# Kernel tuning notes

Hardware: AMD Instinct MI355X
Metric: run time of the kernel (lower is better)

Reference implementation:

```python
import jax, jax.numpy as jnp
import numpy as np

B, S, H = 2, 2048, 1024
NUM_HEAD = 16
HEAD = H // NUM_HEAD
NEG = -10000000000.0


def setup_inputs() -> dict:
    key = jax.random.key(0)
    ks = jax.random.split(key, 10)
    scale = 1.0 / np.sqrt(H)
    return {
        "query": jax.random.normal(ks[0], (B, S, H), jnp.float32),
        "key": jax.random.normal(ks[1], (B, S, H), jnp.float32),
        "value": jax.random.normal(ks[2], (B, S, H), jnp.float32),
        "mask": jax.random.randint(ks[3], (B, S), 0, 2, jnp.int32),
        "Wq": jax.random.normal(ks[4], (H, H), jnp.float32) * scale,
        "bq": jnp.zeros((H,), jnp.float32),
        "Wk": jax.random.normal(ks[5], (H, H), jnp.float32) * scale,
        "bk": jnp.zeros((H,), jnp.float32),
        "Wv": jax.random.normal(ks[6], (H, H), jnp.float32) * scale,
        "bv": jnp.zeros((H,), jnp.float32),
    }


def reference(query, key, value, mask, Wq, bq, Wk, bk, Wv, bv):
    b, s, h = query.shape
    # Linear projections (torch Linear: x @ W.T + b), split into heads -> [b, nh, s, hd]
    def proj(x, W, bias):
        y = x @ W.T + bias
        return y.reshape(b, s, NUM_HEAD, HEAD).transpose(0, 2, 1, 3)

    q = proj(query, Wq, bq)
    k = proj(key, Wk, bk)
    v = proj(value, Wv, bv)

    # NOTE: original module has NO 1/sqrt(head_dim) scaling -- faithful.
    attn_score = jnp.einsum("bhqd,bhkd->bhqk", q, k)  # [b, nh, s, s]
    # key-padding mask bias: 0 where mask==1, -1e10 where mask==0, broadcast over query dim
    bias_add = jnp.where(mask[:, None, None, :] == 0, NEG, 0.0).astype(attn_score.dtype)
    attn_score = attn_score + bias_add
    attn_ratio = jax.nn.softmax(attn_score, axis=-1)
    out = jnp.einsum("bhqk,bhkd->bhqd", attn_ratio, v)  # [b, nh, s, hd]
    out = out.transpose(0, 2, 1, 3).reshape(b, s, h)
    # Dropout is identity in eval mode; output_linear is defined but never used in forward.
    return out
```

## Files before the change

kernel.cpp:

```cpp
#include <hip/hip_runtime.h>

#define BATCH 2
#define S_LEN 2048
#define HDIM  1024
#define NHEAD 16
#define HD    64
#define NEGBIAS -1e10f
#define LOG2E 1.44269504088896f

typedef __attribute__((ext_vector_type(8))) _Float16 half8;
typedef __attribute__((ext_vector_type(4))) _Float16 half4;
typedef __attribute__((ext_vector_type(4))) float   f32x4;
typedef __attribute__((ext_vector_type(2))) __fp16 fp16x2;
typedef __attribute__((ext_vector_type(4))) __fp16 fp16x4;
typedef __attribute__((ext_vector_type(8))) __fp16 fp16x8;

__device__ __forceinline__ float max3f(float a, float b, float c) {
    return fmaxf(fmaxf(a, b), c);
}

__global__ __launch_bounds__(256) void proj_gemm_f16(
    const float* __restrict__ Xq, const float* __restrict__ Wq, const float* __restrict__ bq,
    const float* __restrict__ Xk, const float* __restrict__ Wk, const float* __restrict__ bk,
    const float* __restrict__ Xv, const float* __restrict__ Wv, const float* __restrict__ bv,
    _Float16* __restrict__ Qb, _Float16* __restrict__ Kb, _Float16* __restrict__ Vtb)
{
    const int z = blockIdx.z;
    const float* X    = (z == 0) ? Xq : (z == 1) ? Xk : Xv;
    const float* W    = (z == 0) ? Wq : (z == 1) ? Wk : Wv;
    const float* bias = (z == 0) ? bq : (z == 1) ? bk : bv;
    _Float16* Y       = (z == 0) ? Qb : (z == 1) ? Kb : Vtb;

    const int n0 = blockIdx.x * 128;
    const int m0 = blockIdx.y * 128;

    __shared__ __align__(16) _Float16 As[128][40];
    __shared__ __align__(16) _Float16 Bs[128][40];

    const int t    = threadIdx.x;
    const int w    = t >> 6;
    const int lane = t & 63;
    const int quad = lane >> 4;
    const int lc   = lane & 15;
    const int wm   = (w >> 1) * 64;
    const int wn   = (w & 1) * 64;

    const f32x4 fzero = {0.f, 0.f, 0.f, 0.f};
    f32x4 acc[4][4];
#pragma unroll
    for (int i = 0; i < 4; i++)
#pragma unroll
        for (int j = 0; j < 4; j++) acc[i][j] = fzero;

    const int srow = t >> 2;
    const int sc   = t & 3;

    float4 xa[2][2], wa[2][2];
#define PROJ_ISSUE(K0)                                                        \
    {                                                                         \
        _Pragma("unroll")                                                     \
        for (int hf = 0; hf < 2; hf++) {                                      \
            const float* gx = X + (size_t)(m0 + srow + hf * 64) * HDIM + (K0) + sc * 8; \
            xa[hf][0] = *(const float4*)gx;                                   \
            xa[hf][1] = *(const float4*)(gx + 4);                             \
            const float* gw = W + (size_t)(n0 + srow + hf * 64) * HDIM + (K0) + sc * 8; \
            wa[hf][0] = *(const float4*)gw;                                   \
            wa[hf][1] = *(const float4*)(gw + 4);                             \
        }                                                                     \
    }

#define PK8(dst, f0, f1)                                                      \
    {                                                                         \
        fp16x2 p0 = __builtin_amdgcn_cvt_pkrtz((f0).x, (f0).y);               \
        fp16x2 p1 = __builtin_amdgcn_cvt_pkrtz((f0).z, (f0).w);               \
        fp16x2 p2 = __builtin_amdgcn_cvt_pkrtz((f1).x, (f1).y);               \
        fp16x2 p3 = __builtin_amdgcn_cvt_pkrtz((f1).z, (f1).w);               \
        fp16x4 lo = __builtin_shufflevector(p0, p1, 0, 1, 2, 3);              \
        fp16x4 hi = __builtin_shufflevector(p2, p3, 0, 1, 2, 3);              \
        fp16x8 v8 = __builtin_shufflevector(lo, hi, 0, 1, 2, 3, 4, 5, 6, 7);  \
        dst = __builtin_bit_cast(half8, v8);                                  \
    }

    PROJ_ISSUE(0)

    for (int k0 = 0; k0 < HDIM; k0 += 32) {
        if (k0) __syncthreads();
#pragma unroll
        for (int hf = 0; hf < 2; hf++) {
            int row = srow + hf * 64;
            half8 vx, vw;
            PK8(vx, xa[hf][0], xa[hf][1])
            PK8(vw, wa[hf][0], wa[hf][1])
            *(half8*)&As[row][sc * 8] = vx;
            *(half8*)&Bs[row][sc * 8] = vw;
        }
        __syncthreads();

        if (k0 + 32 < HDIM) PROJ_ISSUE(k0 + 32)

        half8 af[4], bf[4];
#pragma unroll
        for (int mt = 0; mt < 4; mt++)
            af[mt] = *(const half8*)&As[wm + mt * 16 + lc][quad * 8];
#pragma unroll
        for (int nt = 0; nt < 4; nt++)
            bf[nt] = *(const half8*)&Bs[wn + nt * 16 + lc][quad * 8];
#pragma unroll
        for (int mt = 0; mt < 4; mt++)
#pragma unroll
            for (int nt = 0; nt < 4; nt++)
                acc[mt][nt] = __builtin_amdgcn_mfma_f32_16x16x32_f16(
                    af[mt], bf[nt], acc[mt][nt], 0, 0, 0);
    }

#pragma unroll
    for (int nt = 0; nt < 4; nt++) {
        const int n = n0 + wn + nt * 16 + lc;
        const float bv_ = bias[n];
        const int h = n >> 6, d = n & 63;
#pragma unroll
        for (int mt = 0; mt < 4; mt++) {
#pragma unroll
            for (int r = 0; r < 4; r++) {
                const int m = m0 + wm + mt * 16 + quad * 4 + r;
                const int b = m >> 11, s = m & (S_LEN - 1);
                const int bh = b * NHEAD + h;
                float y = acc[mt][nt][r] + bv_;
                if (z == 0) y *= LOG2E;
                _Float16 val = (_Float16)y;
                if (z == 2)
                    Y[((size_t)bh * HD + d) * S_LEN + s] = val;
                else
                    Y[((size_t)bh * S_LEN + s) * HD + d] = val;
            }
        }
    }
}

__global__ __launch_bounds__(256) void flash_attn_mfma(
    const _Float16* __restrict__ Qb, const _Float16* __restrict__ Kb,
    const _Float16* __restrict__ Vtb, const int* __restrict__ mask,
    float* __restrict__ out)
{
    const int bid = blockIdx.x;
    const int swz = (bid & 7) * 64 + (bid >> 3);
    const int qt = swz & 15;
    const int bh = swz >> 4;
    const int b  = bh >> 4;
    const int h  = bh & (NHEAD - 1);

    __shared__ __align__(16) _Float16 Ks [64][72];
    __shared__ __align__(16) _Float16 Vts[64][72];
    __shared__ __align__(16) _Float16 Ps [4][32][72];
    __shared__ float biasS[64];

    const int t    = threadIdx.x;
    const int w    = t >> 6;
    const int lane = t & 63;
    const int quad = lane >> 4;
    const int lc   = lane & 15;

    const _Float16* Kbase = Kb  + (size_t)bh * S_LEN * HD;
    const _Float16* Vbase = Vtb + (size_t)bh * HD * S_LEN;
    const int* mbase = mask + b * S_LEN;

    half8 qf[2][2];
#pragma unroll
    for (int qg = 0; qg < 2; qg++) {
        const int qrow = qt * 128 + w * 32 + qg * 16 + lc;
#pragma unroll
        for (int s = 0; s < 2; s++)
            qf[qg][s] = *(const half8*)(Qb + ((size_t)bh * S_LEN + qrow) * HD
                                        + s * 32 + quad * 8);
    }

    f32x4 o[2][4];
    const f32x4 fzero = {0.f, 0.f, 0.f, 0.f};
#pragma unroll
    for (int qg = 0; qg < 2; qg++)
#pragma unroll
        for (int nt = 0; nt < 4; nt++) o[qg][nt] = fzero;
    float mrun[2] = {-3.0e38f, -3.0e38f};
    float lrun[2] = {0.f, 0.f};

    const int rr0 = t >> 3,          cc0 = (t & 7) * 8;
    const int rr1 = (t + 256) >> 3;

    half8 kpre[2], vpre[2];
    int   mpre;
#define ATTN_ISSUE(KT)                                                        \
    {                                                                         \
        kpre[0] = *(const half8*)(Kbase + (size_t)((KT) + rr0) * HD + cc0);   \
        kpre[1] = *(const half8*)(Kbase + (size_t)((KT) + rr1) * HD + cc0);   \
        vpre[0] = *(const half8*)(Vbase + (size_t)rr0 * S_LEN + (KT) + cc0);  \
        vpre[1] = *(const half8*)(Vbase + (size_t)rr1 * S_LEN + (KT) + cc0);  \
        mpre    = mbase[(KT) + (t & 63)];                                     \
    }

    ATTN_ISSUE(0)

    for (int kt = 0; kt < S_LEN; kt += 64) {
        if (kt) __syncthreads();
        *(half8*)&Ks [rr0][cc0] = kpre[0];
        *(half8*)&Ks [rr1][cc0] = kpre[1];
        *(half8*)&Vts[rr0][cc0] = vpre[0];
        *(half8*)&Vts[rr1][cc0] = vpre[1];
        if (t < 64) biasS[t] = mpre ? 0.f : NEGBIAS;
        __syncthreads();

        if (kt + 64 < S_LEN) ATTN_ISSUE(kt + 64)

        f32x4 scf[2][4];
#pragma unroll
        for (int tt = 0; tt < 4; tt++) {
            float4 b4 = *(const float4*)&biasS[tt * 16 + quad * 4];
            f32x4 cini = {b4.x, b4.y, b4.z, b4.w};
            scf[0][tt] = cini;
            scf[1][tt] = cini;
        }
#pragma unroll
        for (int s = 0; s < 2; s++) {
#pragma unroll
            for (int tt = 0; tt < 4; tt++) {
                half8 kf = *(const half8*)&Ks[tt * 16 + lc][s * 32 + quad * 8];
                scf[0][tt] = __builtin_amdgcn_mfma_f32_16x16x32_f16(kf, qf[0][s], scf[0][tt], 0, 0, 0);
                scf[1][tt] = __builtin_amdgcn_mfma_f32_16x16x32_f16(kf, qf[1][s], scf[1][tt], 0, 0, 0);
            }
        }

#pragma unroll
        for (int qg = 0; qg < 2; qg++) {
            const f32x4 a0 = scf[qg][0], a1 = scf[qg][1],
                        a2 = scf[qg][2], a3 = scf[qg][3];
            float m0 = max3f(a0[0], a0[1], a0[2]);
            float m1 = max3f(a0[3], a1[0], a1[1]);
            float m2 = max3f(a1[2], a1[3], a2[0]);
            float m3 = max3f(a2[1], a2[2], a2[3]);
            float m4 = max3f(a3[0], a3[1], a3[2]);
            float mx = fmaxf(max3f(m0, m1, m2), max3f(m3, m4, a3[3]));
            mx = fmaxf(mx, __shfl_xor(mx, 16));
            mx = fmaxf(mx, __shfl_xor(mx, 32));

            if (!__all(mx <= mrun[qg] + 8.f)) {
                float mn = fmaxf(mrun[qg], mx);
                float al = __builtin_amdgcn_exp2f(mrun[qg] - mn);
                lrun[qg] *= al;
#pragma unroll
                for (int nt = 0; nt < 4; nt++) {
                    o[qg][nt][0] *= al; o[qg][nt][1] *= al;
                    o[qg][nt][2] *= al; o[qg][nt][3] *= al;
                }
                mrun[qg] = mn;
            }

            const float mr = mrun[qg];
            float ps[4][4];
#pragma unroll
            for (int tt = 0; tt < 4; tt++)
#pragma unroll
                for (int r = 0; r < 4; r++) {
                    float p = __builtin_amdgcn_exp2f(scf[qg][tt][r] - mr);
                    ps[tt][r] = p;
                }
            float s0 = (ps[0][0] + ps[0][1]) + (ps[0][2] + ps[0][3]);
            float s1 = (ps[1][0] + ps[1][1]) + (ps[1][2] + ps[1][3]);
            float s2 = (ps[2][0] + ps[2][1]) + (ps[2][2] + ps[2][3]);
            float s3 = (ps[3][0] + ps[3][1]) + (ps[3][2] + ps[3][3]);
            float ls = (s0 + s1) + (s2 + s3);
            ls += __shfl_xor(ls, 16);
            ls += __shfl_xor(ls, 32);
            lrun[qg] += ls;

#pragma unroll
            for (int tt = 0; tt < 4; tt++) {
                fp16x2 p01 = __builtin_amdgcn_cvt_pkrtz(ps[tt][0], ps[tt][1]);
                fp16x2 p23 = __builtin_amdgcn_cvt_pkrtz(ps[tt][2], ps[tt][3]);
                fp16x4 pk4 = __builtin_shufflevector(p01, p23, 0, 1, 2, 3);
                *(half4*)&Ps[w][qg * 16 + lc][tt * 16 + quad * 4] =
                    __builtin_bit_cast(half4, pk4);
            }
        }

#pragma unroll
        for (int s = 0; s < 2; s++) {
            half8 pf0 = *(const half8*)&Ps[w][lc]     [s * 32 + quad * 8];
            half8 pf1 = *(const half8*)&Ps[w][16 + lc][s * 32 + quad * 8];
#pragma unroll
            for (int nt = 0; nt < 4; nt++) {
                half8 vf = *(const half8*)&Vts[nt * 16 + lc][s * 32 + quad * 8];
                o[0][nt] = __builtin_amdgcn_mfma_f32_16x16x32_f16(vf, pf0, o[0][nt], 0, 0, 0);
                o[1][nt] = __builtin_amdgcn_mfma_f32_16x16x32_f16(vf, pf1, o[1][nt], 0, 0, 0);
            }
        }
    }

#pragma unroll
    for (int qg = 0; qg < 2; qg++) {
        const int qrow = qt * 128 + w * 32 + qg * 16 + lc;
        const float inv = 1.f / lrun[qg];
        const size_t rowb = ((size_t)b * S_LEN + qrow) * HDIM + h * HD;
#pragma unroll
        for (int nt = 0; nt < 4; nt++) {
            float4 v;
            v.x = o[qg][nt][0] * inv; v.y = o[qg][nt][1] * inv;
            v.z = o[qg][nt][2] * inv; v.w = o[qg][nt][3] * inv;
            *(float4*)&out[rowb + nt * 16 + quad * 4] = v;
        }
    }
}

extern "C" void kernel_launch(void* const* d_in, const int* in_sizes, int n_in,
                              void* d_out, int out_size, void* d_ws, size_t ws_size,
                              hipStream_t stream) {
    const float* query = (const float*)d_in[0];
    const float* key   = (const float*)d_in[1];
    const float* value = (const float*)d_in[2];
    const int*   mask  = (const int*)  d_in[3];
    const float* Wq    = (const float*)d_in[4];
    const float* bq    = (const float*)d_in[5];
    const float* Wk    = (const float*)d_in[6];
    const float* bk    = (const float*)d_in[7];
    const float* Wv    = (const float*)d_in[8];
    const float* bv    = (const float*)d_in[9];
    float* out = (float*)d_out;

    const size_t nElem = (size_t)BATCH * S_LEN * HDIM;
    if (ws_size < 3 * nElem * sizeof(_Float16)) return;
    _Float16* Qb  = (_Float16*)d_ws;
    _Float16* Kb  = Qb + nElem;
    _Float16* Vtb = Kb + nElem;

    dim3 gproj(HDIM / 128, (BATCH * S_LEN) / 128, 3);
    proj_gemm_f16<<<gproj, 256, 0, stream>>>(query, Wq, bq, key, Wk, bk,
                                             value, Wv, bv, Qb, Kb, Vtb);

    flash_attn_mfma<<<BATCH * NHEAD * (S_LEN / 128), 256, 0, stream>>>(
        Qb, Kb, Vtb, mask, out);
}
```

Before: 234.4 us.

## Remap projection grid for XCD locality and double-buffer global prefetch

The projection GEMM now runs on a flat 1D grid of 768 blocks. The block index is remapped so that consecutive blocks landing on the same XCD (l&7) share M tiles and nearby N tiles, which should improve L2 reuse of X and W. The K loop now keeps two register prefetch buffers, so global loads are issued two stages ahead, hiding more memory latency. The cost is more registers, which may lower occupancy.

```diff
diff --git a/kernel.cpp b/kernel.cpp
--- a/kernel.cpp
+++ b/kernel.cpp
@@ -25,14 +25,20 @@
     const float* __restrict__ Xv, const float* __restrict__ Wv, const float* __restrict__ bv,
     _Float16* __restrict__ Qb, _Float16* __restrict__ Kb, _Float16* __restrict__ Vtb)
 {
-    const int z = blockIdx.z;
+    const int l  = blockIdx.x;
+    const int x  = l & 7;
+    const int j  = l >> 3;
+    const int mt_ = x * 4 + (j & 3);
+    const int nt_ = (j >> 2) & 7;
+    const int z   = j >> 5;
+
     const float* X    = (z == 0) ? Xq : (z == 1) ? Xk : Xv;
     const float* W    = (z == 0) ? Wq : (z == 1) ? Wk : Wv;
     const float* bias = (z == 0) ? bq : (z == 1) ? bk : bv;
     _Float16* Y       = (z == 0) ? Qb : (z == 1) ? Kb : Vtb;
 
-    const int n0 = blockIdx.x * 128;
-    const int m0 = blockIdx.y * 128;
+    const int n0 = nt_ * 128;
+    const int m0 = mt_ * 128;
 
     __shared__ __align__(16) _Float16 As[128][40];
     __shared__ __align__(16) _Float16 Bs[128][40];
@@ -50,22 +56,23 @@
 #pragma unroll
     for (int i = 0; i < 4; i++)
 #pragma unroll
-        for (int j = 0; j < 4; j++) acc[i][j] = fzero;
+        for (int j2 = 0; j2 < 4; j2++) acc[i][j2] = fzero;
 
     const int srow = t >> 2;
     const int sc   = t & 3;
 
-    float4 xa[2][2], wa[2][2];
-#define PROJ_ISSUE(K0)                                                        \
+    float4 xa0[2][2], wa0[2][2], xa1[2][2], wa1[2][2];
+
+#define PROJ_ISSUE(K0, XA, WA)                                                \
     {                                                                         \
         _Pragma("unroll")                                                     \
         for (int hf = 0; hf < 2; hf++) {                                      \
             const float* gx = X + (size_t)(m0 + srow + hf * 64) * HDIM + (K0) + sc * 8; \
-            xa[hf][0] = *(const float4*)gx;                                   \
-            xa[hf][1] = *(const float4*)(gx + 4);                             \
+            XA[hf][0] = *(const float4*)gx;                                   \
+            XA[hf][1] = *(const float4*)(gx + 4);                             \
             const float* gw = W + (size_t)(n0 + srow + hf * 64) * HDIM + (K0) + sc * 8; \
-            wa[hf][0] = *(const float4*)gw;                                   \
-            wa[hf][1] = *(const float4*)(gw + 4);                             \
+            WA[hf][0] = *(const float4*)gw;                                   \
+            WA[hf][1] = *(const float4*)(gw + 4);                             \
         }                                                                     \
     }
 
@@ -81,36 +88,51 @@
         dst = __builtin_bit_cast(half8, v8);                                  \
     }
 
-    PROJ_ISSUE(0)
-
-    for (int k0 = 0; k0 < HDIM; k0 += 32) {
+#define PROJ_STAGE(XA, WA)                                                    \
+    {                                                                         \
+        _Pragma("unroll")                                                     \
+        for (int hf = 0; hf < 2; hf++) {                                      \
+            int row = srow + hf * 64;                                         \
+            half8 vx, vw;                                                     \
+            PK8(vx, XA[hf][0], XA[hf][1])                                     \
+            PK8(vw, WA[hf][0], WA[hf][1])                                     \
+            *(half8*)&As[row][sc * 8] = vx;                                   \
+            *(half8*)&Bs[row][sc * 8] = vw;                                   \
+        }                                                                     \
+    }
+
+#define PROJ_COMPUTE                                                          \
+    {                                                                         \
+        half8 af[4], bf[4];                                                   \
+        _Pragma("unroll")                                                     \
+        for (int mt = 0; mt < 4; mt++)                                        \
+            af[mt] = *(const half8*)&As[wm + mt * 16 + lc][quad * 8];         \
+        _Pragma("unroll")                                                     \
+        for (int nt = 0; nt < 4; nt++)                                        \
+            bf[nt] = *(const half8*)&Bs[wn + nt * 16 + lc][quad * 8];         \
+        _Pragma("unroll")                                                     \
+        for (int mt = 0; mt < 4; mt++)                                        \
+            _Pragma("unroll")                                                 \
+            for (int nt = 0; nt < 4; nt++)                                    \
+                acc[mt][nt] = __builtin_amdgcn_mfma_f32_16x16x32_f16(         \
+                    af[mt], bf[nt], acc[mt][nt], 0, 0, 0);                    \
+    }
+
+    PROJ_ISSUE(0,  xa0, wa0)
+    PROJ_ISSUE(32, xa1, wa1)
+
+    for (int k0 = 0; k0 < HDIM; k0 += 64) {
         if (k0) __syncthreads();
-#pragma unroll
-        for (int hf = 0; hf < 2; hf++) {
-            int row = srow + hf * 64;
-            half8 vx, vw;
-            PK8(vx, xa[hf][0], xa[hf][1])
-            PK8(vw, wa[hf][0], wa[hf][1])
-            *(half8*)&As[row][sc * 8] = vx;
-            *(half8*)&Bs[row][sc * 8] = vw;
-        }
+        PROJ_STAGE(xa0, wa0)
         __syncthreads();
-
-        if (k0 + 32 < HDIM) PROJ_ISSUE(k0 + 32)
-
-        half8 af[4], bf[4];
-#pragma unroll
-        for (int mt = 0; mt < 4; mt++)
-            af[mt] = *(const half8*)&As[wm + mt * 16 + lc][quad * 8];
-#pragma unroll
-        for (int nt = 0; nt < 4; nt++)
-            bf[nt] = *(const half8*)&Bs[wn + nt * 16 + lc][quad * 8];
-#pragma unroll
-        for (int mt = 0; mt < 4; mt++)
-#pragma unroll
-            for (int nt = 0; nt < 4; nt++)
-                acc[mt][nt] = __builtin_amdgcn_mfma_f32_16x16x32_f16(
-                    af[mt], bf[nt], acc[mt][nt], 0, 0, 0);
+        if (k0 + 64 < HDIM) PROJ_ISSUE(k0 + 64, xa0, wa0)
+        PROJ_COMPUTE
+
+        __syncthreads();
+        PROJ_STAGE(xa1, wa1)
+        __syncthreads();
+        if (k0 + 96 < HDIM) PROJ_ISSUE(k0 + 96, xa1, wa1)
+        PROJ_COMPUTE
     }
 
 #pragma unroll
@@ -330,9 +352,8 @@
     _Float16* Kb  = Qb + nElem;
     _Float16* Vtb = Kb + nElem;
 
-    dim3 gproj(HDIM / 128, (BATCH * S_LEN) / 128, 3);
-    proj_gemm_f16<<<gproj, 256, 0, stream>>>(query, Wq, bq, key, Wk, bk,
-                                             value, Wv, bv, Qb, Kb, Vtb);
+    proj_gemm_f16<<<768, 256, 0, stream>>>(query, Wq, bq, key, Wk, bk,
+                                           value, Wv, bv, Qb, Kb, Vtb);
 
     flash_attn_mfma<<<BATCH * NHEAD * (S_LEN / 128), 256, 0, stream>>>(
         Qb, Kb, Vtb, mask, out);
```

After: 236.3 us. No clear change (+0.8%).

## Load K/V fragments directly from global memory, dropping shared-memory staging and block barriers

Applied to the files above, without the earlier changes.

The attention kernel no longer stages K, V^T and the mask bias through shared memory with a register prefetch and two __syncthreads per tile. Each wave now loads its MFMA K and V fragments and its mask values straight from global memory, relying on L1/L2 to serve the data that the four waves share. It also raises wave priority around the MFMA blocks with s_setprio. This removes barriers and LDS traffic but gives up explicit prefetch overlap, so each wave issues redundant global loads whose latency may be exposed.

```diff
diff --git a/kernel.cpp b/kernel.cpp
--- a/kernel.cpp
+++ b/kernel.cpp
@@ -17,6 +17,17 @@
 
 __device__ __forceinline__ float max3f(float a, float b, float c) {
     return fmaxf(fmaxf(a, b), c);
+}
+
+__device__ __forceinline__ half8 pk8(float4 a, float4 b) {
+    fp16x2 p0 = __builtin_amdgcn_cvt_pkrtz(a.x, a.y);
+    fp16x2 p1 = __builtin_amdgcn_cvt_pkrtz(a.z, a.w);
+    fp16x2 p2 = __builtin_amdgcn_cvt_pkrtz(b.x, b.y);
+    fp16x2 p3 = __builtin_amdgcn_cvt_pkrtz(b.z, b.w);
+    fp16x4 lo = __builtin_shufflevector(p0, p1, 0, 1, 2, 3);
+    fp16x4 hi = __builtin_shufflevector(p2, p3, 0, 1, 2, 3);
+    fp16x8 v8 = __builtin_shufflevector(lo, hi, 0, 1, 2, 3, 4, 5, 6, 7);
+    return __builtin_bit_cast(half8, v8);
 }
 
 __global__ __launch_bounds__(256) void proj_gemm_f16(
@@ -50,7 +61,7 @@
 #pragma unroll
     for (int i = 0; i < 4; i++)
 #pragma unroll
-        for (int j = 0; j < 4; j++) acc[i][j] = fzero;
+        for (int j2 = 0; j2 < 4; j2++) acc[i][j2] = fzero;
 
     const int srow = t >> 2;
     const int sc   = t & 3;
@@ -69,18 +80,6 @@
         }                                                                     \
     }
 
-#define PK8(dst, f0, f1)                                                      \
-    {                                                                         \
-        fp16x2 p0 = __builtin_amdgcn_cvt_pkrtz((f0).x, (f0).y);               \
-        fp16x2 p1 = __builtin_amdgcn_cvt_pkrtz((f0).z, (f0).w);               \
-        fp16x2 p2 = __builtin_amdgcn_cvt_pkrtz((f1).x, (f1).y);               \
-        fp16x2 p3 = __builtin_amdgcn_cvt_pkrtz((f1).z, (f1).w);               \
-        fp16x4 lo = __builtin_shufflevector(p0, p1, 0, 1, 2, 3);              \
-        fp16x4 hi = __builtin_shufflevector(p2, p3, 0, 1, 2, 3);              \
-        fp16x8 v8 = __builtin_shufflevector(lo, hi, 0, 1, 2, 3, 4, 5, 6, 7);  \
-        dst = __builtin_bit_cast(half8, v8);                                  \
-    }
-
     PROJ_ISSUE(0)
 
     for (int k0 = 0; k0 < HDIM; k0 += 32) {
@@ -88,11 +87,8 @@
 #pragma unroll
         for (int hf = 0; hf < 2; hf++) {
             int row = srow + hf * 64;
-            half8 vx, vw;
-            PK8(vx, xa[hf][0], xa[hf][1])
-            PK8(vw, wa[hf][0], wa[hf][1])
-            *(half8*)&As[row][sc * 8] = vx;
-            *(half8*)&Bs[row][sc * 8] = vw;
+            *(half8*)&As[row][sc * 8] = pk8(xa[hf][0], xa[hf][1]);
+            *(half8*)&Bs[row][sc * 8] = pk8(wa[hf][0], wa[hf][1]);
         }
         __syncthreads();
 
@@ -149,10 +145,7 @@
     const int b  = bh >> 4;
     const int h  = bh & (NHEAD - 1);
 
-    __shared__ __align__(16) _Float16 Ks [64][72];
-    __shared__ __align__(16) _Float16 Vts[64][72];
-    __shared__ __align__(16) _Float16 Ps [4][32][72];
-    __shared__ float biasS[64];
+    __shared__ __align__(16) _Float16 Ps[4][32][72];
 
     const int t    = threadIdx.x;
     const int w    = t >> 6;
@@ -160,9 +153,9 @@
     const int quad = lane >> 4;
     const int lc   = lane & 15;
 
-    const _Float16* Kbase = Kb  + (size_t)bh * S_LEN * HD;
-    const _Float16* Vbase = Vtb + (size_t)bh * HD * S_LEN;
-    const int* mbase = mask + b * S_LEN;
+    const _Float16* Kl = Kb  + (size_t)bh * S_LEN * HD + (size_t)lc * HD + quad * 8;
+    const _Float16* Vl = Vtb + (size_t)bh * HD * S_LEN + (size_t)lc * S_LEN + quad * 8;
+    const int*      ml = mask + b * S_LEN + quad * 4;
 
     half8 qf[2][2];
 #pragma unroll
@@ -183,50 +176,42 @@
     float mrun[2] = {-3.0e38f, -3.0e38f};
     float lrun[2] = {0.f, 0.f};
 
-    const int rr0 = t >> 3,          cc0 = (t & 7) * 8;
-    const int rr1 = (t + 256) >> 3;
-
-    half8 kpre[2], vpre[2];
-    int   mpre;
-#define ATTN_ISSUE(KT)                                                        \
-    {                                                                         \
-        kpre[0] = *(const half8*)(Kbase + (size_t)((KT) + rr0) * HD + cc0);   \
-        kpre[1] = *(const half8*)(Kbase + (size_t)((KT) + rr1) * HD + cc0);   \
-        vpre[0] = *(const half8*)(Vbase + (size_t)rr0 * S_LEN + (KT) + cc0);  \
-        vpre[1] = *(const half8*)(Vbase + (size_t)rr1 * S_LEN + (KT) + cc0);  \
-        mpre    = mbase[(KT) + (t & 63)];                                     \
-    }
-
-    ATTN_ISSUE(0)
-
     for (int kt = 0; kt < S_LEN; kt += 64) {
-        if (kt) __syncthreads();
-        *(half8*)&Ks [rr0][cc0] = kpre[0];
-        *(half8*)&Ks [rr1][cc0] = kpre[1];
-        *(half8*)&Vts[rr0][cc0] = vpre[0];
-        *(half8*)&Vts[rr1][cc0] = vpre[1];
-        if (t < 64) biasS[t] = mpre ? 0.f : NEGBIAS;
-        __syncthreads();
-
-        if (kt + 64 < S_LEN) ATTN_ISSUE(kt + 64)
+        int4 mm[4];
+#pragma unroll
+        for (int tt = 0; tt < 4; tt++)
+            mm[tt] = *(const int4*)(ml + kt + tt * 16);
+
+        half8 vfr[2][4];
+#pragma unroll
+        for (int s = 0; s < 2; s++)
+#pragma unroll
+            for (int nt = 0; nt < 4; nt++)
+                vfr[s][nt] = *(const half8*)(Vl + (size_t)(nt * 16) * S_LEN
+                                             + kt + s * 32);
 
         f32x4 scf[2][4];
 #pragma unroll
         for (int tt = 0; tt < 4; tt++) {
-            float4 b4 = *(const float4*)&biasS[tt * 16 + quad * 4];
-            f32x4 cini = {b4.x, b4.y, b4.z, b4.w};
+            f32x4 cini;
+            cini[0] = mm[tt].x ? 0.f : NEGBIAS;
+            cini[1] = mm[tt].y ? 0.f : NEGBIAS;
+            cini[2] = mm[tt].z ? 0.f : NEGBIAS;
+            cini[3] = mm[tt].w ? 0.f : NEGBIAS;
             scf[0][tt] = cini;
             scf[1][tt] = cini;
         }
+        __builtin_amdgcn_s_setprio(1);
 #pragma unroll
         for (int s = 0; s < 2; s++) {
 #pragma unroll
             for (int tt = 0; tt < 4; tt++) {
-                half8 kf = *(const half8*)&Ks[tt * 16 + lc][s * 32 + quad * 8];
+                half8 kf = *(const half8*)(Kl + (size_t)(kt + tt * 16) * HD + s * 32);
                 scf[0][tt] = __builtin_amdgcn_mfma_f32_16x16x32_f16(kf, qf[0][s], scf[0][tt], 0, 0, 0);
                 scf[1][tt] = __builtin_amdgcn_mfma_f32_16x16x32_f16(kf, qf[1][s], scf[1][tt], 0, 0, 0);
             }
         }
+        __builtin_amdgcn_s_setprio(0);
 
 #pragma unroll
         for (int qg = 0; qg < 2; qg++) {
@@ -281,17 +266,18 @@
             }
         }
 
+        __builtin_amdgcn_s_setprio(1);
 #pragma unroll
         for (int s = 0; s < 2; s++) {
             half8 pf0 = *(const half8*)&Ps[w][lc]     [s * 32 + quad * 8];
             half8 pf1 = *(const half8*)&Ps[w][16 + lc][s * 32 + quad * 8];
 #pragma unroll
             for (int nt = 0; nt < 4; nt++) {
-                half8 vf = *(const half8*)&Vts[nt * 16 + lc][s * 32 + quad * 8];
-                o[0][nt] = __builtin_amdgcn_mfma_f32_16x16x32_f16(vf, pf0, o[0][nt], 0, 0, 0);
-                o[1][nt] = __builtin_amdgcn_mfma_f32_16x16x32_f16(vf, pf1, o[1][nt], 0, 0, 0);
-            }
-        }
+                o[0][nt] = __builtin_amdgcn_mfma_f32_16x16x32_f16(vfr[s][nt], pf0, o[0][nt], 0, 0, 0);
+                o[1][nt] = __builtin_amdgcn_mfma_f32_16x16x32_f16(vfr[s][nt], pf1, o[1][nt], 0, 0, 0);
+            }
+        }
+        __builtin_amdgcn_s_setprio(0);
     }
 
 #pragma unroll
```

After: 307.1 us. 1.31x slower.
